# Kernel optimization log

Hardware: AMD Instinct MI355X
Metric: run time of the kernel (lower is better)

## Reference

```python
import math
import jax, jax.numpy as jnp
import numpy as np

B, L, C, H = 32, 320, 768, 12
LENS_T = 64
KEEP_RATIO = 0.7
AD_H = 64   # Mixer adapter bottleneck width (assumed bottleneck adapter)
EPS = 1e-5  # torch LayerNorm default


def _ln(x, g, b):
    m = jnp.mean(x, axis=-1, keepdims=True)
    v = jnp.mean((x - m) ** 2, axis=-1, keepdims=True)
    return (x - m) * jax.lax.rsqrt(v + EPS) * g + b


def _attention(x, qkv_w, proj_w, proj_b):
    b, l, c = x.shape
    dh = c // H
    qkv = (x @ qkv_w).reshape(b, l, 3, H, dh)
    q = jnp.transpose(qkv[:, :, 0], (0, 2, 1, 3))  # [B,H,L,Dh]
    k = jnp.transpose(qkv[:, :, 1], (0, 2, 1, 3))
    v = jnp.transpose(qkv[:, :, 2], (0, 2, 1, 3))
    a = jax.nn.softmax(jnp.einsum('bhid,bhjd->bhij', q * (dh ** -0.5), k), axis=-1)
    out = jnp.einsum('bhij,bhjd->bhid', a, v).transpose(0, 2, 1, 3).reshape(b, l, c)
    return out @ proj_w + proj_b, a


def _mixer(x, dw, db, uw, ub):
    return jax.nn.gelu(x @ dw + db, approximate=False) @ uw + ub


def _mlp(x, w1, b1, w2, b2):
    return jax.nn.gelu(x @ w1 + b1, approximate=False) @ w2 + b2


def _ce(attn, tokens, lens_t, lens_keep, gidx):
    # attn: [B,H,Lt+Ls,Lt+Ls]; average template->search block over heads and template rows
    attn_t = jnp.mean(attn[:, :, :lens_t, lens_t:], axis=(1, 2))  # [B, Ls]
    order = jnp.argsort(-attn_t, axis=1)                          # descending sort indices
    topk_idx, rest_idx = order[:, :lens_keep], order[:, lens_keep:]
    keep = jnp.take_along_axis(gidx, topk_idx, axis=1)
    removed = jnp.take_along_axis(gidx, rest_idx, axis=1)
    kept_tok = jnp.take_along_axis(tokens[:, lens_t:], topk_idx[..., None], axis=1)
    return jnp.concatenate([tokens[:, :lens_t], kept_tok], axis=1), keep, removed


def setup_inputs():
    key = jax.random.key(0)
    ks = jax.random.split(key, 12)
    p = lambda k, shape: jax.random.normal(k, shape, jnp.float32) * 0.02
    ls = L - LENS_T
    return {
        'x': jax.random.normal(ks[0], (B, L, C), jnp.float32),
        'xi': jax.random.normal(ks[1], (B, L, C), jnp.float32),
        'gi_t': jnp.arange(B * LENS_T, dtype=jnp.int32).reshape(B, LENS_T),
        'gi_ti': jnp.arange(B * LENS_T, dtype=jnp.int32).reshape(B, LENS_T),
        'gi_s': jnp.arange(B * ls, dtype=jnp.int32).reshape(B, ls),
        'gi_si': jnp.arange(B * ls, dtype=jnp.int32).reshape(B, ls),
        'layer': 0,
        'n1_g': jnp.ones((C,), jnp.float32), 'n1_b': jnp.zeros((C,), jnp.float32),
        'qkv_w': p(ks[2], (C, 3 * C)),
        'proj_w': p(ks[3], (C, C)), 'proj_b': jnp.zeros((C,), jnp.float32),
        'n2_g': jnp.ones((C,), jnp.float32), 'n2_b': jnp.zeros((C,), jnp.float32),
        'fc1_w': p(ks[4], (C, 4 * C)), 'fc1_b': jnp.zeros((4 * C,), jnp.float32),
        'fc2_w': p(ks[5], (4 * C, C)), 'fc2_b': jnp.zeros((C,), jnp.float32),
        'ad1_dw': p(ks[6], (C, AD_H)), 'ad1_db': jnp.zeros((AD_H,), jnp.float32),
        'ad1_uw': p(ks[7], (AD_H, C)), 'ad1_ub': jnp.zeros((C,), jnp.float32),
        'ad2_dw': p(ks[8], (C, AD_H)), 'ad2_db': jnp.zeros((AD_H,), jnp.float32),
        'ad2_uw': p(ks[9], (AD_H, C)), 'ad2_ub': jnp.zeros((C,), jnp.float32),
    }


def reference(x, xi, gi_t, gi_ti, gi_s, gi_si, layer,
              n1_g, n1_b, qkv_w, proj_w, proj_b, n2_g, n2_b,
              fc1_w, fc1_b, fc2_w, fc2_b,
              ad1_dw, ad1_db, ad1_uw, ad1_ub, ad2_dw, ad2_db, ad2_uw, ad2_ub):
    # layer not in {3,6,9}: Mixer-adapter path, then candidate elimination, then MLP
    xori = x
    xa, attn = _attention(_ln(x, n1_g, n1_b), qkv_w, proj_w, proj_b)
    x = x + xa + _mixer(_ln(xi, n1_g, n1_b), ad1_dw, ad1_db, ad1_uw, ad1_ub)
    xia, i_attn = _attention(_ln(xi, n1_g, n1_b), qkv_w, proj_w, proj_b)
    xi = xi + xia + _mixer(_ln(xori, n1_g, n1_b), ad1_dw, ad1_db, ad1_uw, ad1_ub)
    lens_t = gi_t.shape[1]
    lens_s = x.shape[1] - lens_t
    lens_keep = math.ceil(KEEP_RATIO * lens_s)  # 180
    x, gi_s, removed = _ce(attn, x, lens_t, lens_keep, gi_s)
    xi, gi_si, removedi = _ce(i_attn, xi, lens_t, lens_keep, gi_si)
    xori = x
    x = x + _mlp(_ln(x, n2_g, n2_b), fc1_w, fc1_b, fc2_w, fc2_b) \
          + _mixer(_ln(xi, n2_g, n2_b), ad2_dw, ad2_db, ad2_uw, ad2_ub)
    xi = xi + _mlp(_ln(xi, n2_g, n2_b), fc1_w, fc1_b, fc2_w, fc2_b) \
            + _mixer(_ln(xori, n2_g, n2_b), ad2_dw, ad2_db, ad2_uw, ad2_ub)
    return (x, gi_t, gi_s, removed, attn, xi, gi_ti, gi_si, removedi, i_attn)
```

## Files before the change

kernel.cpp:

```cpp
#include <hip/hip_runtime.h>
#include <hip/hip_bf16.h>

#define NB   32
#define LL   320
#define CC   768
#define NH   12
#define DHD  64
#define LT   64
#define LSN  256
#define NKEEP 180
#define NREM  76
#define LP   244
#define ADH  64
#define C4   3072

typedef __attribute__((ext_vector_type(8))) short s16x8;
typedef __attribute__((ext_vector_type(4))) float f32x4;

__device__ __forceinline__ ushort f2b(float f){
  union { __hip_bfloat16 h; ushort u; } cv;
  cv.h = __float2bfloat16(f);
  return cv.u;
}

__device__ __forceinline__ void glds16(const ushort* g, ushort* l){
  __builtin_amdgcn_global_load_lds(
      (const __attribute__((address_space(1))) void*)g,
      (__attribute__((address_space(3))) void*)l, 16, 0, 0);
}

__device__ __forceinline__ float blk_sum(float v, float* sh){
  #pragma unroll
  for (int o = 32; o > 0; o >>= 1) v += __shfl_down(v, o, 64);
  int w = threadIdx.x >> 6;
  if ((threadIdx.x & 63) == 0) sh[w] = v;
  __syncthreads();
  float r = sh[0] + sh[1] + sh[2] + sh[3];
  __syncthreads();
  return r;
}

__global__ __launch_bounds__(256) void ln12_k(const float* __restrict__ x0,
                                              const float* __restrict__ x1,
                                              int rowsplit,
                                              const float* __restrict__ g,
                                              const float* __restrict__ be,
                                              float* __restrict__ y,
                                              ushort* __restrict__ yb,
                                              float* __restrict__ lnt){
  __shared__ float sh[4];
  int row = blockIdx.x;
  const float* xr = (row < rowsplit) ? x0 + (size_t)row * CC
                                     : x1 + (size_t)(row - rowsplit) * CC;
  int t = threadIdx.x;
  float v0 = xr[t], v1 = xr[t + 256], v2 = xr[t + 512];
  float m = blk_sum(v0 + v1 + v2, sh) * (1.0f / 768.0f);
  float d0 = v0 - m, d1 = v1 - m, d2 = v2 - m;
  float var = blk_sum(d0*d0 + d1*d1 + d2*d2, sh) * (1.0f / 768.0f);
  float rs = rsqrtf(var + 1e-5f);
  float o0 = d0 * rs * g[t]       + be[t];
  float o1 = d1 * rs * g[t + 256] + be[t + 256];
  float o2 = d2 * rs * g[t + 512] + be[t + 512];
  float* yr = y + (size_t)row * CC;
  yr[t] = o0; yr[t + 256] = o1; yr[t + 512] = o2;
  if (yb){
    ushort* yr2 = yb + (size_t)row * CC;
    yr2[t] = f2b(o0); yr2[t + 256] = f2b(o1); yr2[t + 512] = f2b(o2);
  }
  if (lnt){
    int i = row % LL;
    if (i < 64){
      float* lr = lnt + ((size_t)(row / LL) * 64 + i) * CC;
      lr[t] = o0; lr[t + 256] = o1; lr[t + 512] = o2;
    }
  }
}

__device__ __forceinline__ void f32gemm_body(
    float* As, float* Bs, int bx, int by,
    const float* __restrict__ A1, const float* __restrict__ W1,
    float* __restrict__ C1, ushort* __restrict__ Cb1,
    const float* __restrict__ A2, const float* __restrict__ W2,
    float* __restrict__ C2,
    int K, int ldw, int ldc, int ysplit)
{
  const int t = threadIdx.x;
  const int tx = t & 15, ty = t >> 4;
  const int n0 = bx * 128;
  const float* A; const float* W; float* Cm; ushort* Cb; int m0;
  if (by < ysplit){ A = A1; W = W1; Cm = C1; Cb = Cb1; m0 = by * 128; }
  else            { A = A2; W = W2; Cm = C2; Cb = nullptr; m0 = (by - ysplit) * 128; }

  float acc[8][8] = {};
  for (int k0 = 0; k0 < K; k0 += 32){
    #pragma unroll
    for (int q = 0; q < 4; q++){
      int idx = t + q*256;
      int m = idx & 127, kq = idx >> 7;
      float4 v = *reinterpret_cast<const float4*>(A + (size_t)(m0+m)*K + k0 + kq*4);
      As[(kq*4+0)*128 + m] = v.x; As[(kq*4+1)*128 + m] = v.y;
      As[(kq*4+2)*128 + m] = v.z; As[(kq*4+3)*128 + m] = v.w;
    }
    #pragma unroll
    for (int q = 0; q < 4; q++){
      int idx = t + q*256;
      int kr = idx >> 5, nq = idx & 31;
      float4 v = *reinterpret_cast<const float4*>(W + (size_t)(k0+kr)*ldw + n0 + nq*4);
      *reinterpret_cast<float4*>(&Bs[kr*128 + nq*4]) = v;
    }
    __syncthreads();
    #pragma unroll
    for (int kk = 0; kk < 32; kk++){
      float a[8], b[8];
      *reinterpret_cast<float4*>(&a[0]) = *reinterpret_cast<float4*>(&As[kk*128 + ty*4]);
      *reinterpret_cast<float4*>(&a[4]) = *reinterpret_cast<float4*>(&As[kk*128 + 64 + ty*4]);
      *reinterpret_cast<float4*>(&b[0]) = *reinterpret_cast<float4*>(&Bs[kk*128 + tx*4]);
      *reinterpret_cast<float4*>(&b[4]) = *reinterpret_cast<float4*>(&Bs[kk*128 + 64 + tx*4]);
      #pragma unroll
      for (int i = 0; i < 8; i++)
        #pragma unroll
        for (int j = 0; j < 8; j++)
          acc[i][j] = fmaf(a[i], b[j], acc[i][j]);
    }
    __syncthreads();
  }
  #pragma unroll
  for (int i = 0; i < 8; i++){
    int m = m0 + ty*4 + (i & 3) + (i >> 2) * 64;
    #pragma unroll
    for (int j = 0; j < 8; j++){
      int n = n0 + tx*4 + (j & 3) + (j >> 2) * 64;
      float v = acc[i][j];
      Cm[(size_t)m * ldc + n] = v;
      if (Cb) Cb[(size_t)m * ldc + n] = f2b(v);
    }
  }
}

template<bool GELU, bool ACC, bool OBF>
__device__ __forceinline__ void mg_body(
    ushort* Asm, ushort* Bsm, int bx, int by,
    const ushort* __restrict__ A, const ushort* __restrict__ Wt,
    const float* __restrict__ bias, void* __restrict__ Cp,
    int M, int N, int K,
    const float* __restrict__ res0, const float* __restrict__ res1, int Mhalf,
    const ushort* __restrict__ A2_0, const ushort* __restrict__ A2_1,
    const ushort* __restrict__ W2t, int K2, const float* __restrict__ bias2,
    void* __restrict__ Cp1)
{
  const int t = threadIdx.x;
  const int m0 = by * 128, n0 = bx * 128;
  const int wave = t >> 6, lane = t & 63;
  const int wrow = wave >> 1, wcol = wave & 1;
  const int lr = lane & 15, ks = lane >> 4;
  const int srow = lane >> 2, scp = lane & 3;

  f32x4 acc[4][4];
  #pragma unroll
  for (int i = 0; i < 4; i++)
    #pragma unroll
    for (int j = 0; j < 4; j++)
      #pragma unroll
      for (int r = 0; r < 4; r++) acc[i][j][r] = 0.f;

  const int nseg = W2t ? 2 : 1;
  for (int seg = 0; seg < nseg; seg++){
    const ushort* Abase; const ushort* Bbase; int ldA, ldB, Ks;
    if (seg == 0){
      Abase = A + (size_t)m0 * K; ldA = K; Bbase = Wt; ldB = K; Ks = K;
    } else {
      Abase = (res1 && m0 >= Mhalf) ? (A2_1 + (size_t)(m0 - Mhalf) * K2)
                                    : (A2_0 + (size_t)m0 * K2);
      ldA = K2; Bbase = W2t; ldB = K2; Ks = K2;
    }
    for (int k0 = 0; k0 < Ks; k0 += 32){
      #pragma unroll
      for (int q = 0; q < 2; q++){
        int r16 = wave*32 + q*16;
        int row = r16 + srow;
        int sch = scp ^ ((row >> 1) & 3);
        glds16(Abase + (size_t)row * ldA + k0 + sch*8, &Asm[r16*32]);
        int rbn = n0 + row; if (rbn > N-1) rbn = N-1;
        glds16(Bbase + (size_t)rbn * ldB + k0 + sch*8, &Bsm[r16*32]);
      }
      __syncthreads();
      s16x8 af[4], bf[4];
      #pragma unroll
      for (int f = 0; f < 4; f++){
        int ra = wrow*64 + f*16 + lr;
        af[f] = *reinterpret_cast<const s16x8*>(&Asm[ra*32 + ((ks ^ ((ra>>1)&3))<<3)]);
        int rbn = wcol*64 + f*16 + lr;
        bf[f] = *reinterpret_cast<const s16x8*>(&Bsm[rbn*32 + ((ks ^ ((rbn>>1)&3))<<3)]);
      }
      #pragma unroll
      for (int i = 0; i < 4; i++)
        #pragma unroll
        for (int j = 0; j < 4; j++)
          acc[i][j] = __builtin_amdgcn_mfma_f32_16x16x32_bf16(af[i], bf[j], acc[i][j], 0, 0, 0);
      __syncthreads();
    }
  }
  #pragma unroll
  for (int i = 0; i < 4; i++){
    int mb = m0 + wrow*64 + i*16 + ks*4;
    #pragma unroll
    for (int j = 0; j < 4; j++){
      int n = n0 + wcol*64 + j*16 + lr;
      if (n >= N) continue;
      float bv = (bias ? bias[n] : 0.0f) + (bias2 ? bias2[n] : 0.0f);
      #pragma unroll
      for (int r = 0; r < 4; r++){
        int mrow = mb + r;
        float v = acc[i][j][r] + bv;
        if (GELU) v = 0.5f * v * (1.0f + erff(v * 0.70710678118654752f));
        if (res0){
          if (res1 && mrow >= Mhalf) v += res1[(size_t)(mrow - Mhalf) * N + n];
          else                       v += res0[(size_t)mrow * N + n];
        }
        if (Cp1 && mrow >= Mhalf){
          size_t idx = (size_t)(mrow - Mhalf) * N + n;
          if (OBF)      ((ushort*)Cp1)[idx] = f2b(v);
          else if (ACC) ((float*)Cp1)[idx] += v;
          else          ((float*)Cp1)[idx]  = v;
        } else {
          size_t idx = (size_t)mrow * N + n;
          if (OBF)      ((ushort*)Cp)[idx] = f2b(v);
          else if (ACC) ((float*)Cp)[idx] += v;
          else          ((float*)Cp)[idx]  = v;
        }
      }
    }
  }
}

template<bool GELU, bool ACC, bool OBF>
__global__ __launch_bounds__(256) void mg_k(
    const ushort* __restrict__ A, const ushort* __restrict__ Wt,
    const float* __restrict__ bias, void* __restrict__ Cp,
    int M, int N, int K,
    const float* __restrict__ res0, const float* __restrict__ res1, int Mhalf,
    const ushort* __restrict__ A2_0, const ushort* __restrict__ A2_1,
    const ushort* __restrict__ W2t, int K2, const float* __restrict__ bias2,
    void* __restrict__ Cp1)
{
  __shared__ __align__(16) ushort shm[8192];
  mg_body<GELU,ACC,OBF>(shm, shm + 4096, blockIdx.x, blockIdx.y,
                        A, Wt, bias, Cp, M, N, K, res0, res1, Mhalf,
                        A2_0, A2_1, W2t, K2, bias2, Cp1);
}

#define FA_F32 1152
#define FA_QV  1920
__global__ __launch_bounds__(256) void fuseA_k(
    const float* __restrict__ lnf, const float* __restrict__ qkvw,
    float* __restrict__ kf, ushort* __restrict__ kbm,
    const float* __restrict__ lnt, float* __restrict__ qt,
    const ushort* __restrict__ ln1b, const ushort* __restrict__ Wt_q,
    ushort* __restrict__ qvb,
    const ushort* __restrict__ Wt_a1d, const float* __restrict__ a1db,
    ushort* __restrict__ mixhb)
{
  __shared__ __align__(16) float sh[8192];
  int bid = blockIdx.x;
  if (bid < FA_F32){
    f32gemm_body(sh, sh + 4096, bid % 6, bid / 6,
                 lnf, qkvw + 768, kf, kbm, lnt, qkvw, qt,
                 CC, 2304, CC, 160);
  } else if (bid < FA_F32 + FA_QV){
    int b2 = bid - FA_F32;
    mg_body<false,false,true>((ushort*)sh, (ushort*)sh + 4096, b2 % 12, b2 / 12,
        ln1b, Wt_q, nullptr, qvb, 2*NB*LL, 1536, CC,
        nullptr, nullptr, 0, nullptr, nullptr, nullptr, 0, nullptr, nullptr);
  } else {
    int by = bid - FA_F32 - FA_QV;
    mg_body<true,false,true>((ushort*)sh, (ushort*)sh + 4096, 0, by,
        ln1b, Wt_a1d, a1db, mixhb, 2*NB*LL, ADH, CC,
        nullptr, nullptr, 0, nullptr, nullptr, nullptr, 0, nullptr, nullptr);
  }
}

__global__ __launch_bounds__(256) void fuseB_k(
    const ushort* __restrict__ ln2b, const ushort* __restrict__ Wt_fc1,
    const float* __restrict__ fc1b, ushort* __restrict__ hidb,
    const ushort* __restrict__ Wt_a2d, const float* __restrict__ a2db,
    ushort* __restrict__ mixh2b)
{
  __shared__ __align__(16) ushort shm[8192];
  int bid = blockIdx.x;
  if (bid < 24*122){
    mg_body<true,false,true>(shm, shm + 4096, bid % 24, bid / 24,
        ln2b, Wt_fc1, fc1b, hidb, 2*NB*LP, C4, CC,
        nullptr, nullptr, 0, nullptr, nullptr, nullptr, 0, nullptr, nullptr);
  } else {
    mg_body<true,false,true>(shm, shm + 4096, 0, bid - 24*122,
        ln2b, Wt_a2d, a2db, mixh2b, 2*NB*LP, ADH, CC,
        nullptr, nullptr, 0, nullptr, nullptr, nullptr, 0, nullptr, nullptr);
  }
}

__device__ __forceinline__ void scorest_body(
    float* shf, int jt, int s, int bh,
    const float* __restrict__ qt, const float* __restrict__ kf,
    float* __restrict__ sc)
{
  float* Qs = shf;
  float* Ks = shf + 16*65;
  const int t = threadIdx.x, tx = t & 15, ty = t >> 4;
  const int b = bh / NH, h = bh % NH;
  const int j0 = jt * 64;
  const float* qts = qt + (size_t)s * NB * 64 * CC;
  const float* kfs = kf + (size_t)s * NB * LL * CC;
  const size_t qbase = (size_t)b * 64 * CC + (size_t)h * 64;
  const size_t kbase = (size_t)b * LL * CC + (size_t)h * 64;
  const int lkk = t & 15, lmm = t >> 4;
  float acc[4][4] = {};
  for (int d0 = 0; d0 < DHD; d0 += 16){
    #pragma unroll
    for (int q = 0; q < 4; q++)
      Qs[lkk*65 + lmm + 16*q] = qts[qbase + (size_t)(lmm + 16*q) * CC + d0 + lkk];
    #pragma unroll
    for (int q = 0; q < 4; q++)
      Ks[lkk*65 + lmm + 16*q] = kfs[kbase + (size_t)(j0 + lmm + 16*q) * CC + d0 + lkk];
    __syncthreads();
    #pragma unroll
    for (int kk = 0; kk < 16; kk++){
      float a[4], b2[4];
      #pragma unroll
      for (int i = 0; i < 4; i++) a[i] = Qs[kk*65 + ty*4 + i];
      #pragma unroll
      for (int j = 0; j < 4; j++) b2[j] = Ks[kk*65 + tx*4 + j];
      #pragma unroll
      for (int i = 0; i < 4; i++)
        #pragma unroll
        for (int j = 0; j < 4; j++)
          acc[i][j] = fmaf(a[i], b2[j], acc[i][j]);
    }
    __syncthreads();
  }
  #pragma unroll
  for (int i = 0; i < 4; i++)
    #pragma unroll
    for (int j = 0; j < 4; j++)
      sc[((size_t)bh * LL + ty*4 + i) * LL + j0 + tx*4 + j] = acc[i][j] * 0.125f;
}

__device__ __forceinline__ void sqs_body(
    ushort* Qs, ushort* Ks, int it, int bh, int s,
    const ushort* __restrict__ qv, const ushort* __restrict__ kb,
    float* __restrict__ sc)
{
  const int t = threadIdx.x;
  const int b = bh / NH, h = bh % NH;
  const int w = t >> 6, lane = t & 63;
  const int lr = lane & 15, ks = lane >> 4;
  const int qrow0 = s * NB * LL + b * LL + 64 + it * 64;
  const int krow0 = s * NB * LL + b * LL;

  #pragma unroll
  for (int q = 0; q < 4; q++){
    int idx = t + q*256;
    int row = idx >> 4, dv = idx & 15;
    *reinterpret_cast<ushort4*>(&Qs[row*72 + dv*4]) =
      *reinterpret_cast<const ushort4*>(qv + (size_t)(qrow0 + row) * 1536 + h*64 + dv*4);
  }

  f32x4 acc[5][4];
  #pragma unroll
  for (int jt = 0; jt < 5; jt++)
    #pragma unroll
    for (int n = 0; n < 4; n++)
      #pragma unroll
      for (int r = 0; r < 4; r++) acc[jt][n][r] = 0.f;

  for (int jt = 0; jt < 5; jt++){
    __syncthreads();
    #pragma unroll
    for (int q = 0; q < 4; q++){
      int idx = t + q*256;
      int row = idx >> 4, dv = idx & 15;
      *reinterpret_cast<ushort4*>(&Ks[row*72 + dv*4]) =
        *reinterpret_cast<const ushort4*>(kb + (size_t)(krow0 + jt*64 + row) * CC + h*64 + dv*4);
    }
    __syncthreads();
    #pragma unroll
    for (int n = 0; n < 4; n++)
      #pragma unroll
      for (int kt = 0; kt < 2; kt++){
        s16x8 a  = *reinterpret_cast<const s16x8*>(&Qs[(w*16 + lr)*72 + kt*32 + ks*8]);
        s16x8 bb = *reinterpret_cast<const s16x8*>(&Ks[(n*16 + lr)*72 + kt*32 + ks*8]);
        acc[jt][n] = __builtin_amdgcn_mfma_f32_16x16x32_bf16(a, bb, acc[jt][n], 0, 0, 0);
      }
  }
  #pragma unroll
  for (int jt = 0; jt < 5; jt++)
    #pragma unroll
    for (int n = 0; n < 4; n++)
      #pragma unroll
      for (int r = 0; r < 4; r++) acc[jt][n][r] *= 0.125f;
  #pragma unroll
  for (int r = 0; r < 4; r++){
    float mx = -3.4e38f;
    #pragma unroll
    for (int jt = 0; jt < 5; jt++)
      #pragma unroll
      for (int n = 0; n < 4; n++) mx = fmaxf(mx, acc[jt][n][r]);
    #pragma unroll
    for (int o = 1; o < 16; o <<= 1) mx = fmaxf(mx, __shfl_xor(mx, o, 64));
    float sum = 0.f;
    #pragma unroll
    for (int jt = 0; jt < 5; jt++)
      #pragma unroll
      for (int n = 0; n < 4; n++){
        float e = expf(acc[jt][n][r] - mx);
        acc[jt][n][r] = e; sum += e;
      }
    #pragma unroll
    for (int o = 1; o < 16; o <<= 1) sum += __shfl_xor(sum, o, 64);
    float inv = 1.0f / sum;
    size_t rowbase = ((size_t)bh * LL + 64 + it*64 + w*16 + ks*4 + r) * LL;
    #pragma unroll
    for (int jt = 0; jt < 5; jt++)
      #pragma unroll
      for (int n = 0; n < 4; n++)
        sc[rowbase + jt*64 + n*16 + lr] = acc[jt][n][r] * inv;
  }
}

#define SC_T 3840
__global__ __launch_bounds__(256) void scoresf_k(
    const float* __restrict__ qt, const float* __restrict__ kf,
    const ushort* __restrict__ qv, const ushort* __restrict__ kb,
    float* __restrict__ p0, float* __restrict__ p1)
{
  __shared__ __align__(16) ushort shm[2*64*72];
  int bid = blockIdx.x;
  if (bid < SC_T){
    int jt = bid % 5; int r = bid / 5; int s = r & 1; int bh = r >> 1;
    scorest_body((float*)shm, jt, s, bh, qt, kf, s ? p1 : p0);
  } else {
    int b2 = bid - SC_T;
    int it = b2 & 3; int r = b2 >> 2; int bh = r % (NB*NH); int s = r / (NB*NH);
    sqs_body(shm, shm + 64*72, it, bh, s, qv, kb, s ? p1 : p0);
  }
}

__global__ __launch_bounds__(256) void softmaxt_k(float* __restrict__ p0,
                                                  float* __restrict__ p1,
                                                  double* __restrict__ pp){
  __shared__ float a4[4][256];
  const int lane = threadIdx.x & 63;
  const int w = threadIdx.x >> 6;
  const int s = blockIdx.x / (NB*NH*16);
  const int bx = blockIdx.x % (NB*NH*16);
  const int bh = bx >> 4;
  const int i0 = (bx & 15) * 4;
  float* sc = s ? p1 : p0;
  const size_t row = (size_t)bh * LL + i0 + w;
  float* sr = sc + row * LL;
  float v[5]; float mx = -3.4e38f;
  #pragma unroll
  for (int i = 0; i < 5; i++){ v[i] = sr[lane + 64*i]; mx = fmaxf(mx, v[i]); }
  #pragma unroll
  for (int o = 32; o > 0; o >>= 1) mx = fmaxf(mx, __shfl_xor(mx, o, 64));
  float s2 = 0.f;
  #pragma unroll
  for (int i = 0; i < 5; i++){ v[i] = expf(v[i] - mx); s2 += v[i]; }
  #pragma unroll
  for (int o = 32; o > 0; o >>= 1) s2 += __shfl_xor(s2, o, 64);
  float inv = 1.0f / s2;
  #pragma unroll
  for (int i = 0; i < 5; i++){
    float p = v[i] * inv;
    sr[lane + 64*i] = p;
    if (i >= 1) a4[w][lane + 64*(i-1)] = p;
  }
  __syncthreads();
  int t = threadIdx.x;
  double ssum = ((double)a4[0][t] + (double)a4[1][t])
              + ((double)a4[2][t] + (double)a4[3][t]);
  double s0 = (double)a4[0][t];
  s0 += (double)a4[1][t]; s0 += (double)a4[2][t]; s0 += (double)a4[3][t];
  (void)ssum;
  pp[(size_t)blockIdx.x * 256 + t] = s0;
}

__global__ __launch_bounds__(256) void attnt2_k(const double* __restrict__ pp,
                                                float* __restrict__ at){
  int g = blockIdx.x;
  int s = g / NB, b = g % NB;
  int j = threadIdx.x;
  double sum = 0.0;
  for (int h = 0; h < NH; h++)
    for (int p = 0; p < 16; p++)
      sum += pp[((size_t)(s*NB*NH + b*NH + h) * 16 + p) * 256 + j];
  at[g * LSN + j] = (float)(sum * (1.0 / 768.0));
}

__global__ __launch_bounds__(256) void pvm_k(const float* __restrict__ p0,
                                             const float* __restrict__ p1,
                                             const ushort* __restrict__ qv,
                                             ushort* __restrict__ pvb){
  __shared__ ushort Pa[64][72];
  __shared__ ushort Vt[64][72];
  const int t = threadIdx.x;
  const int bh = blockIdx.y, s = blockIdx.z;
  const int b = bh / NH, h = bh % NH;
  const int i0 = blockIdx.x * 64;
  const int w = t >> 6, lane = t & 63;
  const int lr = lane & 15, ks = lane >> 4;
  const float* Ap = (s ? p1 : p0) + (size_t)bh * LL * LL;
  const int vrow0 = s * NB * LL + b * LL;
  ushort* pvs = pvb + (size_t)s * NB * LL * CC;

  f32x4 acc[4];
  #pragma unroll
  for (int n = 0; n < 4; n++)
    #pragma unroll
    for (int r = 0; r < 4; r++) acc[n][r] = 0.f;

  for (int jt = 0; jt < 5; jt++){
    int j0 = jt * 64;
    #pragma unroll
    for (int q = 0; q < 4; q++){
      int idx = t + q*256;
      int i = idx >> 4, jv = idx & 15;
      float4 v = *reinterpret_cast<const float4*>(Ap + (size_t)(i0 + i) * LL + j0 + jv*4);
      ushort4 u; u.x = f2b(v.x); u.y = f2b(v.y); u.z = f2b(v.z); u.w = f2b(v.w);
      *reinterpret_cast<ushort4*>(&Pa[i][jv*4]) = u;
    }
    #pragma unroll
    for (int q = 0; q < 4; q++){
      int idx = t + q*256;
      int j = idx >> 4, dv = idx & 15;
      ushort4 u = *reinterpret_cast<const ushort4*>(
          qv + (size_t)(vrow0 + j0 + j) * 1536 + 768 + h*64 + dv*4);
      Vt[dv*4+0][j] = u.x; Vt[dv*4+1][j] = u.y;
      Vt[dv*4+2][j] = u.z; Vt[dv*4+3][j] = u.w;
    }
    __syncthreads();
    #pragma unroll
    for (int n = 0; n < 4; n++)
      #pragma unroll
      for (int kt = 0; kt < 2; kt++){
        s16x8 a = *reinterpret_cast<const s16x8*>(&Pa[w*16 + lr][kt*32 + ks*8]);
        s16x8 bb = *reinterpret_cast<const s16x8*>(&Vt[n*16 + lr][kt*32 + ks*8]);
        acc[n] = __builtin_amdgcn_mfma_f32_16x16x32_bf16(a, bb, acc[n], 0, 0, 0);
      }
    __syncthreads();
  }
  #pragma unroll
  for (int n = 0; n < 4; n++)
    #pragma unroll
    for (int r = 0; r < 4; r++){
      int i = w*16 + ks*4 + r;
      int d = n*16 + lr;
      pvs[(size_t)(b * LL + i0 + i) * 768 + h*64 + d] = f2b(acc[n][r]);
    }
}

__global__ __launch_bounds__(256) void ce_rank_k(const float* __restrict__ at,
                                                 int* __restrict__ ordbuf){
  __shared__ float a[256];
  __shared__ int ord[256];
  int b = blockIdx.x, t = threadIdx.x;
  a[t] = at[b * LSN + t];
  ord[t] = t;
  __syncthreads();
  float mine = a[t];
  int rank = 0;
  for (int k = 0; k < 256; k++){
    float ak = a[k];
    rank += (ak > mine) || (ak == mine && k < t);
  }
  if (rank >= 0 && rank < 256) ord[rank] = t;
  __syncthreads();
  ordbuf[(size_t)b * LSN + t] = ord[t];
}

__global__ __launch_bounds__(256) void ce_emit2_k(const int* __restrict__ ordbuf,
                                                  const int* __restrict__ g0,
                                                  const int* __restrict__ g1,
                                                  const int* __restrict__ t0,
                                                  const int* __restrict__ t1,
                                                  float* __restrict__ keep0,
                                                  float* __restrict__ keep1,
                                                  float* __restrict__ rem0,
                                                  float* __restrict__ rem1,
                                                  float* __restrict__ git0,
                                                  float* __restrict__ git1){
  int g = blockIdx.x, t = threadIdx.x;
  int s = g / NB, b = g % NB;
  const int* gidx = s ? g1 : g0;
  const int* gt   = s ? t1 : t0;
  float* out_keep = s ? keep1 : keep0;
  float* out_rem  = s ? rem1 : rem0;
  float* out_git  = s ? git1 : git0;
  int o = ordbuf[(size_t)g * LSN + t];
  o = min(max(o, 0), 255);
  int idx = gidx[b * LSN + o];
  if (t < NKEEP) out_keep[b * NKEEP + t] = (float)idx;
  else           out_rem[b * NREM + (t - NKEEP)] = (float)idx;
  if (t < LT)    out_git[b * LT + t] = (float)gt[b * LT + t];
}

__global__ __launch_bounds__(256) void gather_k(const float* __restrict__ xnew,
                                                const int* __restrict__ ordbuf,
                                                float* __restrict__ x2){
  int g = blockIdx.x;
  int s = g / (NB*LP), r0 = g % (NB*LP);
  int b = r0 / LP, r = r0 % LP;
  int o = (r < LT) ? 0 : ordbuf[(size_t)(s*NB + b) * LSN + (r - LT)];
  o = min(max(o, 0), 255);
  int src = (r < LT) ? r : (LT + o);
  const float* sp = xnew + (size_t)s * NB * LL * CC + ((size_t)b * LL + src) * CC;
  float* d = x2 + (size_t)s * NB * LP * CC + (size_t)r0 * CC;
  for (int i = threadIdx.x; i < CC; i += 256) d[i] = sp[i];
}

struct TJ { const float* W; ushort* Wt; int K, N, ldw, colOff, blk0; };
struct TJobs { TJ j[9]; };
__global__ __launch_bounds__(256) void tconvm_k(TJobs jobs){
  __shared__ float tile[32][33];
  int bid = blockIdx.x;
  int ji = 0;
  #pragma unroll
  for (int i = 1; i < 9; i++) if (bid >= jobs.j[i].blk0) ji = i;
  TJ jb = jobs.j[ji];
  int local = bid - jb.blk0;
  int txl = jb.N / 32;
  int n0 = (local % txl) * 32, k0 = (local / txl) * 32;
  int t = threadIdx.x;
  int tx = t & 31, ty = t >> 5;
  #pragma unroll
  for (int q = 0; q < 4; q++)
    tile[ty + 8*q][tx] = jb.W[(size_t)(k0 + ty + 8*q) * jb.ldw + jb.colOff + n0 + tx];
  __syncthreads();
  #pragma unroll
  for (int q = 0; q < 4; q++)
    jb.Wt[(size_t)(n0 + ty + 8*q) * jb.K + k0 + tx] = f2b(tile[tx][ty + 8*q]);
}

__global__ void sentinel_k(float* __restrict__ d, float val, int n){
  int i = blockIdx.x * 256 + threadIdx.x;
  if (i < n) d[i] = val;
}

extern "C" void kernel_launch(void* const* d_in, const int* in_sizes, int n_in,
                              void* d_out, int out_size, void* d_ws, size_t ws_size,
                              hipStream_t stream) {
  float* out = (float*)d_out;
  float* ws  = (float*)d_ws;

  static const int EXP[26] = {
    7864320, 7864320, 2048, 2048, 8192, 8192, 1,
    768, 768, 1769472, 589824, 768, 768, 768,
    2359296, 3072, 2359296, 768,
    49152, 64, 49152, 768, 49152, 64, 49152, 768 };

  const void* P[26];
  bool ok = false;
  if (n_in == 26){
    bool m = true; int bad = -1;
    for (int i = 0; i < 26; i++) if (in_sizes[i] != EXP[i]){ m = false; bad = i; break; }
    if (m){ for (int i = 0; i < 26; i++) P[i] = d_in[i]; ok = true; }
    else { sentinel_k<<<16, 256, 0, stream>>>(out, 20000.0f + 16.0f*bad, 4096); return; }
  } else if (n_in == 25){
    bool m = true; int bad = -1;
    for (int i = 0; i < 25; i++){
      int j = (i < 6) ? i : i + 1;
      if (in_sizes[i] != EXP[j]){ m = false; bad = i; break; }
    }
    if (m){
      for (int j = 0; j < 26; j++) P[j] = (j == 6) ? nullptr : d_in[(j < 6) ? j : j - 1];
      ok = true;
    } else { sentinel_k<<<16, 256, 0, stream>>>(out, 20000.0f + 16.0f*bad, 4096); return; }
  }
  if (!ok){ sentinel_k<<<16, 256, 0, stream>>>(out, 10000.0f + 8.0f*n_in, 4096); return; }
  if (out_size != 90656768){
    sentinel_k<<<16, 256, 0, stream>>>(out, 60000.0f + (float)(out_size / 1000000), 4096); return;
  }

  const float* x      = (const float*)P[0];
  const float* xi     = (const float*)P[1];
  const int*   gi_t   = (const int*)P[2];
  const int*   gi_ti  = (const int*)P[3];
  const int*   gi_s   = (const int*)P[4];
  const int*   gi_si  = (const int*)P[5];
  const float* n1_g   = (const float*)P[7];
  const float* n1_b   = (const float*)P[8];
  const float* qkv_w  = (const float*)P[9];
  const float* proj_w = (const float*)P[10];
  const float* proj_b = (const float*)P[11];
  const float* n2_g   = (const float*)P[12];
  const float* n2_b   = (const float*)P[13];
  const float* fc1_w  = (const float*)P[14];
  const float* fc1_b  = (const float*)P[15];
  const float* fc2_w  = (const float*)P[16];
  const float* fc2_b  = (const float*)P[17];
  const float* ad1_dw = (const float*)P[18];
  const float* ad1_db = (const float*)P[19];
  const float* ad1_uw = (const float*)P[20];
  const float* ad1_ub = (const float*)P[21];
  const float* ad2_dw = (const float*)P[22];
  const float* ad2_db = (const float*)P[23];
  const float* ad2_uw = (const float*)P[24];
  const float* ad2_ub = (const float*)P[25];

  const size_t o_x     = 0;
  const size_t o_git   = 5996544;
  const size_t o_gis   = 5998592;
  const size_t o_rem   = 6004352;
  const size_t o_attn  = 6006784;
  const size_t o_xi    = 45328384;
  const size_t o_giti  = 51324928;
  const size_t o_gisi  = 51326976;
  const size_t o_remi  = 51332736;
  const size_t o_iattn = 51335168;

  const size_t BLC      = (size_t)NB * LL * CC;
  const size_t BPC      = (size_t)NB * LP * CC;
  const size_t off_ln   = 0;
  const size_t off_l1b  = off_ln  + 2*BLC;
  const size_t off_k    = off_l1b + BLC;
  const size_t off_qv   = off_k   + 2*BLC;
  const size_t off_kb   = off_qv  + 2*BLC;
  const size_t off_lnt  = off_kb  + BLC;
  const size_t off_qt   = off_lnt + 3145728;
  const size_t off_xnew = off_qt  + 3145728;
  const size_t off_l2b  = off_xnew+ 2*BLC;
  const size_t off_mixh = off_l2b + BPC;
  const size_t off_att  = off_mixh+ 655360;
  const size_t off_attp = off_att + 16384;
  const size_t off_ord  = off_attp+ 6291456;
  const size_t off_wts  = off_ord + 16384;
  const size_t total_f  = off_wts + 3342336;
  if (ws_size < total_f * sizeof(float)){
    sentinel_k<<<16, 256, 0, stream>>>(out, 40000.0f + (float)(ws_size >> 20), 4096);
    return;
  }

  int* ordbuf = (int*)(ws + off_ord);
  double* attp = (double*)(ws + off_attp);
  ushort* wts = (ushort*)(ws + off_wts);
  ushort* Wt_q    = wts;
  ushort* Wt_v    = wts + 589824;
  ushort* Wt_proj = wts + 1179648;
  ushort* Wt_fc1  = wts + 1769472;
  ushort* Wt_fc2  = wts + 4128768;
  ushort* Wt_a1d  = wts + 6488064;
  ushort* Wt_a1u  = wts + 6537216;
  ushort* Wt_a2d  = wts + 6586368;
  ushort* Wt_a2u  = wts + 6635520;
  ushort* ln1b = (ushort*)(ws + off_l1b);
  ushort* qvb  = (ushort*)(ws + off_qv);
  ushort* kb   = (ushort*)(ws + off_kb);
  ushort* pvb  = (ushort*)(ws + off_k);
  ushort* ln2b = (ushort*)(ws + off_l2b);
  ushort* mixhb= (ushort*)(ws + off_mixh);

  float* p0 = out + o_attn;
  float* p1 = out + o_iattn;

  TJobs tj;
  tj.j[0] = { qkv_w,  Wt_q,    768, 768,  2304, 0,    0 };
  tj.j[1] = { qkv_w,  Wt_v,    768, 768,  2304, 1536, 576 };
  tj.j[2] = { proj_w, Wt_proj, 768, 768,  768,  0,    1152 };
  tj.j[3] = { fc1_w,  Wt_fc1,  768, 3072, 3072, 0,    1728 };
  tj.j[4] = { fc2_w,  Wt_fc2,  3072, 768, 768,  0,    4032 };
  tj.j[5] = { ad1_dw, Wt_a1d,  768, 64,   64,   0,    6336 };
  tj.j[6] = { ad1_uw, Wt_a1u,  64,  768,  768,  0,    6384 };
  tj.j[7] = { ad2_dw, Wt_a2d,  768, 64,   64,   0,    6432 };
  tj.j[8] = { ad2_uw, Wt_a2u,  64,  768,  768,  0,    6480 };
  tconvm_k<<<6528, 256, 0, stream>>>(tj);

  ln12_k<<<2*NB*LL, 256, 0, stream>>>(x, xi, NB*LL, n1_g, n1_b,
                                      ws + off_ln, ln1b, ws + off_lnt);

  fuseA_k<<<FA_F32 + FA_QV + 160, 256, 0, stream>>>(
      ws + off_ln, qkv_w, ws + off_k, kb, ws + off_lnt, ws + off_qt,
      ln1b, Wt_q, qvb, Wt_a1d, ad1_db, mixhb);

  scoresf_k<<<SC_T + 3072, 256, 0, stream>>>(ws + off_qt, ws + off_k, qvb, kb, p0, p1);

  softmaxt_k<<<2*NB*NH*16, 256, 0, stream>>>(p0, p1, attp);
  attnt2_k<<<2*NB, 256, 0, stream>>>(attp, ws + off_att);

  pvm_k<<<dim3(5, NB*NH, 2), 256, 0, stream>>>(p0, p1, qvb, pvb);
  mg_k<false,false,false><<<dim3(6, 160), 256, 0, stream>>>(
      pvb, Wt_proj, proj_b, ws + off_xnew, 2*NB*LL, CC, CC,
      x, xi, NB*LL,
      mixhb + (size_t)NB*LL*ADH, mixhb, Wt_a1u, ADH, ad1_ub, nullptr);

  ce_rank_k<<<2*NB, 256, 0, stream>>>(ws + off_att, ordbuf);
  ce_emit2_k<<<2*NB, 256, 0, stream>>>(
      ordbuf, gi_s, gi_si, gi_t, gi_ti,
      out + o_gis, out + o_gisi, out + o_rem, out + o_remi,
      out + o_git, out + o_giti);
  gather_k<<<2*NB*LP, 256, 0, stream>>>(ws + off_xnew, ordbuf, ws + off_ln);

  float* x2  = ws + off_ln;
  float* ln2 = ws + off_xnew;
  ushort* hidb   = (ushort*)(ws + off_k);
  ushort* mixh2b = mixhb;

  ln12_k<<<2*NB*LP, 256, 0, stream>>>(x2, x2, 2*NB*LP, n2_g, n2_b, ln2, ln2b, nullptr);
  fuseB_k<<<24*122 + 122, 256, 0, stream>>>(
      ln2b, Wt_fc1, fc1_b, hidb, Wt_a2d, ad2_db, mixh2b);
  mg_k<false,false,false><<<dim3(6, 122), 256, 0, stream>>>(
      hidb, Wt_fc2, fc2_b, out + o_x, 2*NB*LP, CC, C4,
      x2, x2 + BPC, NB*LP,
      mixh2b + (size_t)NB*LP*ADH, mixh2b, Wt_a2u, ADH, ad2_ub,
      out + o_xi);
}
```

Baseline: 1.367 ms.

## Split fused multi-GEMM and scores kernels back into separate launches

The horizontally fused fuseA_k and scoresf_k kernels are split into separate kernels: an f32 GEMM for K and template Q, a bf16 QV plus adapter kernel, a template-scores kernel and a search-scores MFMA kernel. Each kernel now sizes its own shared memory instead of sharing the largest union buffer, which may raise occupancy for the smaller-footprint parts. The cost is extra launches and lost concurrency between heterogeneous work in a single grid. An unused double-precision sum in the softmax kernel is also removed.

```diff
diff --git a/kernel.cpp b/kernel.cpp
--- a/kernel.cpp
+++ b/kernel.cpp
@@ -76,20 +76,22 @@
   }
 }
 
-__device__ __forceinline__ void f32gemm_body(
-    float* As, float* Bs, int bx, int by,
+__global__ __launch_bounds__(256) void gemm2_k(
     const float* __restrict__ A1, const float* __restrict__ W1,
     float* __restrict__ C1, ushort* __restrict__ Cb1,
     const float* __restrict__ A2, const float* __restrict__ W2,
     float* __restrict__ C2,
     int K, int ldw, int ldc, int ysplit)
 {
+  __shared__ float As[32*128];
+  __shared__ float Bs[32*128];
   const int t = threadIdx.x;
   const int tx = t & 15, ty = t >> 4;
-  const int n0 = bx * 128;
+  const int n0 = blockIdx.x * 128;
+  const int yb = blockIdx.y;
   const float* A; const float* W; float* Cm; ushort* Cb; int m0;
-  if (by < ysplit){ A = A1; W = W1; Cm = C1; Cb = Cb1; m0 = by * 128; }
-  else            { A = A2; W = W2; Cm = C2; Cb = nullptr; m0 = (by - ysplit) * 128; }
+  if (yb < ysplit){ A = A1; W = W1; Cm = C1; Cb = Cb1; m0 = yb * 128; }
+  else            { A = A2; W = W2; Cm = C2; Cb = nullptr; m0 = (yb - ysplit) * 128; }
 
   float acc[8][8] = {};
   for (int k0 = 0; k0 < K; k0 += 32){
@@ -249,36 +251,6 @@
                         A2_0, A2_1, W2t, K2, bias2, Cp1);
 }
 
-#define FA_F32 1152
-#define FA_QV  1920
-__global__ __launch_bounds__(256) void fuseA_k(
-    const float* __restrict__ lnf, const float* __restrict__ qkvw,
-    float* __restrict__ kf, ushort* __restrict__ kbm,
-    const float* __restrict__ lnt, float* __restrict__ qt,
-    const ushort* __restrict__ ln1b, const ushort* __restrict__ Wt_q,
-    ushort* __restrict__ qvb,
-    const ushort* __restrict__ Wt_a1d, const float* __restrict__ a1db,
-    ushort* __restrict__ mixhb)
-{
-  __shared__ __align__(16) float sh[8192];
-  int bid = blockIdx.x;
-  if (bid < FA_F32){
-    f32gemm_body(sh, sh + 4096, bid % 6, bid / 6,
-                 lnf, qkvw + 768, kf, kbm, lnt, qkvw, qt,
-                 CC, 2304, CC, 160);
-  } else if (bid < FA_F32 + FA_QV){
-    int b2 = bid - FA_F32;
-    mg_body<false,false,true>((ushort*)sh, (ushort*)sh + 4096, b2 % 12, b2 / 12,
-        ln1b, Wt_q, nullptr, qvb, 2*NB*LL, 1536, CC,
-        nullptr, nullptr, 0, nullptr, nullptr, nullptr, 0, nullptr, nullptr);
-  } else {
-    int by = bid - FA_F32 - FA_QV;
-    mg_body<true,false,true>((ushort*)sh, (ushort*)sh + 4096, 0, by,
-        ln1b, Wt_a1d, a1db, mixhb, 2*NB*LL, ADH, CC,
-        nullptr, nullptr, 0, nullptr, nullptr, nullptr, 0, nullptr, nullptr);
-  }
-}
-
 __global__ __launch_bounds__(256) void fuseB_k(
     const ushort* __restrict__ ln2b, const ushort* __restrict__ Wt_fc1,
     const float* __restrict__ fc1b, ushort* __restrict__ hidb,
@@ -298,16 +270,36 @@
   }
 }
 
-__device__ __forceinline__ void scorest_body(
-    float* shf, int jt, int s, int bh,
-    const float* __restrict__ qt, const float* __restrict__ kf,
-    float* __restrict__ sc)
+__global__ __launch_bounds__(256) void fuseQVA_k(
+    const ushort* __restrict__ ln1b, const ushort* __restrict__ Wt_q,
+    ushort* __restrict__ qvb,
+    const ushort* __restrict__ Wt_a1d, const float* __restrict__ a1db,
+    ushort* __restrict__ mixhb)
 {
-  float* Qs = shf;
-  float* Ks = shf + 16*65;
+  __shared__ __align__(16) ushort shm[8192];
+  int bid = blockIdx.x;
+  if (bid < 12*160){
+    mg_body<false,false,true>(shm, shm + 4096, bid % 12, bid / 12,
+        ln1b, Wt_q, nullptr, qvb, 2*NB*LL, 1536, CC,
+        nullptr, nullptr, 0, nullptr, nullptr, nullptr, 0, nullptr, nullptr);
+  } else {
+    mg_body<true,false,true>(shm, shm + 4096, 0, bid - 12*160,
+        ln1b, Wt_a1d, a1db, mixhb, 2*NB*LL, ADH, CC,
+        nullptr, nullptr, 0, nullptr, nullptr, nullptr, 0, nullptr, nullptr);
+  }
+}
+
+__global__ __launch_bounds__(256) void scorest_k(const float* __restrict__ qt,
+                                                 const float* __restrict__ kf,
+                                                 float* __restrict__ p0,
+                                                 float* __restrict__ p1){
+  __shared__ float Qs[16][65];
+  __shared__ float Ks[16][65];
   const int t = threadIdx.x, tx = t & 15, ty = t >> 4;
-  const int b = bh / NH, h = bh % NH;
-  const int j0 = jt * 64;
+  const int s = blockIdx.y;
+  const int bh = blockIdx.z; const int b = bh / NH, h = bh % NH;
+  const int j0 = blockIdx.x * 64;
+  float* sc = s ? p1 : p0;
   const float* qts = qt + (size_t)s * NB * 64 * CC;
   const float* kfs = kf + (size_t)s * NB * LL * CC;
   const size_t qbase = (size_t)b * 64 * CC + (size_t)h * 64;
@@ -317,18 +309,18 @@
   for (int d0 = 0; d0 < DHD; d0 += 16){
     #pragma unroll
     for (int q = 0; q < 4; q++)
-      Qs[lkk*65 + lmm + 16*q] = qts[qbase + (size_t)(lmm + 16*q) * CC + d0 + lkk];
+      Qs[lkk][lmm + 16*q] = qts[qbase + (size_t)(lmm + 16*q) * CC + d0 + lkk];
     #pragma unroll
     for (int q = 0; q < 4; q++)
-      Ks[lkk*65 + lmm + 16*q] = kfs[kbase + (size_t)(j0 + lmm + 16*q) * CC + d0 + lkk];
+      Ks[lkk][lmm + 16*q] = kfs[kbase + (size_t)(j0 + lmm + 16*q) * CC + d0 + lkk];
     __syncthreads();
     #pragma unroll
     for (int kk = 0; kk < 16; kk++){
       float a[4], b2[4];
       #pragma unroll
-      for (int i = 0; i < 4; i++) a[i] = Qs[kk*65 + ty*4 + i];
-      #pragma unroll
-      for (int j = 0; j < 4; j++) b2[j] = Ks[kk*65 + tx*4 + j];
+      for (int i = 0; i < 4; i++) a[i] = Qs[kk][ty*4 + i];
+      #pragma unroll
+      for (int j = 0; j < 4; j++) b2[j] = Ks[kk][tx*4 + j];
       #pragma unroll
       for (int i = 0; i < 4; i++)
         #pragma unroll
@@ -344,15 +336,18 @@
       sc[((size_t)bh * LL + ty*4 + i) * LL + j0 + tx*4 + j] = acc[i][j] * 0.125f;
 }
 
-__device__ __forceinline__ void sqs_body(
-    ushort* Qs, ushort* Ks, int it, int bh, int s,
-    const ushort* __restrict__ qv, const ushort* __restrict__ kb,
-    float* __restrict__ sc)
-{
+__global__ __launch_bounds__(256) void sqs_k(const ushort* __restrict__ qv,
+                                             const ushort* __restrict__ kb,
+                                             float* __restrict__ p0,
+                                             float* __restrict__ p1){
+  __shared__ ushort Qs[64][72];
+  __shared__ ushort Ks[64][72];
   const int t = threadIdx.x;
+  const int it = blockIdx.x, bh = blockIdx.y, s = blockIdx.z;
   const int b = bh / NH, h = bh % NH;
   const int w = t >> 6, lane = t & 63;
   const int lr = lane & 15, ks = lane >> 4;
+  float* sc = s ? p1 : p0;
   const int qrow0 = s * NB * LL + b * LL + 64 + it * 64;
   const int krow0 = s * NB * LL + b * LL;
 
@@ -360,7 +355,7 @@
   for (int q = 0; q < 4; q++){
     int idx = t + q*256;
     int row = idx >> 4, dv = idx & 15;
-    *reinterpret_cast<ushort4*>(&Qs[row*72 + dv*4]) =
+    *reinterpret_cast<ushort4*>(&Qs[row][dv*4]) =
       *reinterpret_cast<const ushort4*>(qv + (size_t)(qrow0 + row) * 1536 + h*64 + dv*4);
   }
 
@@ -378,7 +373,7 @@
     for (int q = 0; q < 4; q++){
       int idx = t + q*256;
       int row = idx >> 4, dv = idx & 15;
-      *reinterpret_cast<ushort4*>(&Ks[row*72 + dv*4]) =
+      *reinterpret_cast<ushort4*>(&Ks[row][dv*4]) =
         *reinterpret_cast<const ushort4*>(kb + (size_t)(krow0 + jt*64 + row) * CC + h*64 + dv*4);
     }
     __syncthreads();
@@ -386,8 +381,8 @@
     for (int n = 0; n < 4; n++)
       #pragma unroll
       for (int kt = 0; kt < 2; kt++){
-        s16x8 a  = *reinterpret_cast<const s16x8*>(&Qs[(w*16 + lr)*72 + kt*32 + ks*8]);
-        s16x8 bb = *reinterpret_cast<const s16x8*>(&Ks[(n*16 + lr)*72 + kt*32 + ks*8]);
+        s16x8 a  = *reinterpret_cast<const s16x8*>(&Qs[w*16 + lr][kt*32 + ks*8]);
+        s16x8 bb = *reinterpret_cast<const s16x8*>(&Ks[n*16 + lr][kt*32 + ks*8]);
         acc[jt][n] = __builtin_amdgcn_mfma_f32_16x16x32_bf16(a, bb, acc[jt][n], 0, 0, 0);
       }
   }
@@ -423,24 +418,6 @@
       #pragma unroll
       for (int n = 0; n < 4; n++)
         sc[rowbase + jt*64 + n*16 + lr] = acc[jt][n][r] * inv;
-  }
-}
-
-#define SC_T 3840
-__global__ __launch_bounds__(256) void scoresf_k(
-    const float* __restrict__ qt, const float* __restrict__ kf,
-    const ushort* __restrict__ qv, const ushort* __restrict__ kb,
-    float* __restrict__ p0, float* __restrict__ p1)
-{
-  __shared__ __align__(16) ushort shm[2*64*72];
-  int bid = blockIdx.x;
-  if (bid < SC_T){
-    int jt = bid % 5; int r = bid / 5; int s = r & 1; int bh = r >> 1;
-    scorest_body((float*)shm, jt, s, bh, qt, kf, s ? p1 : p0);
-  } else {
-    int b2 = bid - SC_T;
-    int it = b2 & 3; int r = b2 >> 2; int bh = r % (NB*NH); int s = r / (NB*NH);
-    sqs_body(shm, shm + 64*72, it, bh, s, qv, kb, s ? p1 : p0);
   }
 }
 
@@ -476,11 +453,8 @@
   }
   __syncthreads();
   int t = threadIdx.x;
-  double ssum = ((double)a4[0][t] + (double)a4[1][t])
-              + ((double)a4[2][t] + (double)a4[3][t]);
   double s0 = (double)a4[0][t];
   s0 += (double)a4[1][t]; s0 += (double)a4[2][t]; s0 += (double)a4[3][t];
-  (void)ssum;
   pp[(size_t)blockIdx.x * 256 + t] = s0;
 }
 
@@ -776,11 +750,15 @@
   ln12_k<<<2*NB*LL, 256, 0, stream>>>(x, xi, NB*LL, n1_g, n1_b,
                                       ws + off_ln, ln1b, ws + off_lnt);
 
-  fuseA_k<<<FA_F32 + FA_QV + 160, 256, 0, stream>>>(
-      ws + off_ln, qkv_w, ws + off_k, kb, ws + off_lnt, ws + off_qt,
+  gemm2_k<<<dim3(6, 192), 256, 0, stream>>>(
+      ws + off_ln, qkv_w + 768, ws + off_k, kb,
+      ws + off_lnt, qkv_w, ws + off_qt,
+      CC, 2304, CC, 160);
+  fuseQVA_k<<<12*160 + 160, 256, 0, stream>>>(
       ln1b, Wt_q, qvb, Wt_a1d, ad1_db, mixhb);
 
-  scoresf_k<<<SC_T + 3072, 256, 0, stream>>>(ws + off_qt, ws + off_k, qvb, kb, p0, p1);
+  scorest_k<<<dim3(5, 2, NB*NH), 256, 0, stream>>>(ws + off_qt, ws + off_k, p0, p1);
+  sqs_k<<<dim3(4, NB*NH, 2), 256, 0, stream>>>(qvb, kb, p0, p1);
 
   softmaxt_k<<<2*NB*NH*16, 256, 0, stream>>>(p0, p1, attp);
   attnt2_k<<<2*NB, 256, 0, stream>>>(attp, ws + off_att);
```

New measurement: 1.241 ms, median of 2. 1.1x faster.
